# Optimization experiments

Measured on AMD Instinct MI355X. Metric: run time of the kernel, lower is better.

Reference implementation:

```python
import jax, jax.numpy as jnp
import numpy as np

N = 100000   # num nodes
E = 1200000  # num edges
D = 64       # embedding dim
K = 3        # propagation hops (alpha has K+1 entries)


def setup_inputs() -> dict:
    key = jax.random.key(0)
    k1, k2, k3 = jax.random.split(key, 3)
    edge_index = jax.random.randint(k1, (2, E), 0, N, dtype=jnp.int64)
    weight = jax.random.normal(k2, (N, D), dtype=jnp.float32)
    alpha = jax.random.uniform(k3, (K + 1,), dtype=jnp.float32)
    return {"edge_index": edge_index, "weight": weight, "alpha": alpha}


def reference(edge_index, weight, alpha):
    row = edge_index[0]  # source j
    col = edge_index[1]  # target i
    # symmetric normalization: in-degree over col, deg^-1/2 with inf -> 0
    deg = jax.ops.segment_sum(jnp.ones((E,), dtype=weight.dtype), col, num_segments=N)
    dinv = jnp.where(deg == 0, 0.0, deg ** -0.5)
    edge_w = dinv[row] * dinv[col]  # [E]

    out = weight * alpha[0]
    x = weight
    for k in range(1, K + 1):
        # gather-scale-scatter propagation hop
        msg = edge_w[:, None] * x[row]                      # [E, D]
        x = jax.ops.segment_sum(msg, col, num_segments=N)   # [N, D]
        out = out + x * alpha[k]

    # per-edge link scores: dot(out[src], out[dst])
    return jnp.sum(out[row] * out[col], axis=-1)  # [E]
```

## Files before the change

### kernel.cpp

```cpp
#include <hip/hip_runtime.h>
#include <hip/hip_bf16.h>

#define GN 100000
#define GE 1200000
#define GD 64
#define NG 256
#define CPG 391
#define CAP 6144
#define PADCAP 12032
#define ZROFF (GN << 7)


__global__ void detect_kernel(const void* __restrict__ w,
                              const void* __restrict__ edge,
                              int* __restrict__ flags, int* __restrict__ gcount,
                              __hip_bfloat16* __restrict__ X,
                              __hip_bfloat16* __restrict__ Y) {
    __shared__ int s_badw, s_edgenz;
    if (threadIdx.x == 0) { s_badw = 0; s_edgenz = 0; }
    gcount[threadIdx.x] = 0;
    if (threadIdx.x < 16) {
        uint2 z; z.x = 0u; z.y = 0u;
        *(uint2*)(X + (size_t)GN * GD + 4 * threadIdx.x) = z;
        *(uint2*)(Y + (size_t)GN * GD + 4 * threadIdx.x) = z;
    }
    __syncthreads();
    const unsigned short* wh = (const unsigned short*)w;
    const unsigned int*   ei = (const unsigned int*)edge;
    int badw = 0, edgenz = 0;
    for (int i = threadIdx.x; i < 4096; i += 256) {
        unsigned int bits = ((unsigned int)wh[i]) << 16;
        float v = __uint_as_float(bits);
        if (!(fabsf(v) <= 100.0f)) badw = 1;
        if ((i & 1) == 1 && ei[i] != 0u) edgenz = 1;
    }
    if (badw)   atomicOr(&s_badw, 1);
    if (edgenz) atomicOr(&s_edgenz, 1);
    __syncthreads();
    if (threadIdx.x == 0) {
        flags[0] = s_badw ? 0 : 1;
        flags[1] = s_edgenz ? 0 : 1;
    }
}

__device__ __forceinline__ int ld_row(const int* __restrict__ edge, int e, int e64) {
    return e64 ? edge[2 * (size_t)e] : edge[e];
}
__device__ __forceinline__ int ld_col(const int* __restrict__ edge, int e, int e64) {
    return e64 ? edge[2 * ((size_t)GE + (size_t)e)] : edge[(size_t)GE + (size_t)e];
}
__device__ __forceinline__ float ld_f(const void* __restrict__ p, size_t i, int bf16f) {
    if (bf16f) return __bfloat162float(((const __hip_bfloat16*)p)[i]);
    return ((const float*)p)[i];
}

__device__ __forceinline__ float bf_lo(unsigned u) { return __uint_as_float(u << 16); }
__device__ __forceinline__ float bf_hi(unsigned u) { return __uint_as_float(u & 0xFFFF0000u); }
__device__ __forceinline__ unsigned bf16bits(float f) {
    __hip_bfloat16 h = __float2bfloat16(f);
    unsigned short s;
    __builtin_memcpy(&s, &h, 2);
    return (unsigned)s;
}

__global__ void p1init_kernel(const int* __restrict__ edge, const int* __restrict__ flags,
                              int* __restrict__ gcount, unsigned* __restrict__ bucket,
                              int E, int chunk,
                              const void* __restrict__ w, const void* __restrict__ alpha,
                              __hip_bfloat16* __restrict__ OUT, int nd) {
    if (blockIdx.x < NG) {
        __shared__ int cnt[NG];
        __shared__ int base[NG];
        int t = threadIdx.x;
        int e64 = flags[1];
        cnt[t] = 0;
        __syncthreads();
        int lo = blockIdx.x * chunk;
        int hiE = min(lo + chunk, E);
        for (int e = lo + t; e < hiE; e += 256) {
            int c = ld_col(edge, e, e64);
            int r = ld_row(edge, e, e64);
            if ((unsigned)c < (unsigned)GN && (unsigned)r < (unsigned)GN)
                atomicAdd(&cnt[c / CPG], 1);
        }
        __syncthreads();
        int cv = cnt[t];
        base[t] = (cv > 0) ? atomicAdd(&gcount[t], cv) : 0;
        __syncthreads();
        cnt[t] = 0;
        __syncthreads();
        for (int e = lo + t; e < hiE; e += 256) {
            int c = ld_col(edge, e, e64);
            int r = ld_row(edge, e, e64);
            if ((unsigned)c < (unsigned)GN && (unsigned)r < (unsigned)GN) {
                int g = c / CPG;
                int idx = base[g] + atomicAdd(&cnt[g], 1);
                if (idx < CAP)
                    bucket[(size_t)g * CAP + idx] = ((unsigned)(c - g * CPG) << 17) | (unsigned)r;
            }
        }
    } else {
        int bid = blockIdx.x - NG;
        int i = 4 * (bid * 256 + (int)threadIdx.x);
        int wbf = flags[0];
        if (i < nd) {
            float a0 = ld_f(alpha, 0, wbf);
            float v0 = ld_f(w, i + 0, wbf);
            float v1 = ld_f(w, i + 1, wbf);
            float v2 = ld_f(w, i + 2, wbf);
            float v3 = ld_f(w, i + 3, wbf);
            uint2 oq;
            oq.x = (bf16bits(a0 * v1) << 16) | bf16bits(a0 * v0);
            oq.y = (bf16bits(a0 * v3) << 16) | bf16bits(a0 * v2);
            *(uint2*)(OUT + i) = oq;
        }
    }
}

__global__ void p2_kernel(const unsigned* __restrict__ bucket, const int* __restrict__ gcount,
                          int2* __restrict__ begend, float* __restrict__ dinv,
                          int* __restrict__ csr,
                          const void* __restrict__ w, const int* __restrict__ flags,
                          __hip_bfloat16* __restrict__ XS) {
    int g = blockIdx.x;
    int t = threadIdx.x;
    __shared__ int hist[512];
    __shared__ int s[512];
    __shared__ float sdv[512];
    hist[t] = 0; hist[t + 256] = 0;
    __syncthreads();
    int mg = gcount[g]; if (mg > CAP) mg = CAP;
    const unsigned* bk = bucket + (size_t)g * CAP;
    for (int idx = t; idx < mg; idx += 256)
        atomicAdd(&hist[bk[idx] >> 17], 1);
    __syncthreads();
    int h0 = hist[t], h1 = hist[t + 256];
    int p0 = (h0 + 15) & ~15;
    int p1 = (h1 + 15) & ~15;
    s[t] = p0; s[t + 256] = p1;
    __syncthreads();
    for (int off = 1; off < 512; off <<= 1) {
        int v0 = (t >= off) ? s[t - off] : 0;
        int v1 = (t + 256 >= off) ? s[t + 256 - off] : 0;
        __syncthreads();
        s[t] += v0; s[t + 256] += v1;
        __syncthreads();
    }
    int gb = g * PADCAP;
    int beg0 = gb + s[t] - p0;
    int beg1 = gb + s[t + 256] - p1;
    float dv0 = (h0 > 0) ? rsqrtf((float)h0) : 0.0f;
    float dv1 = (h1 > 0) ? rsqrtf((float)h1) : 0.0f;
    sdv[t] = dv0; sdv[t + 256] = dv1;
    int col0 = g * CPG + t;
    int col1 = col0 + 256;
    if (col0 < GN) {
        begend[col0] = make_int2(beg0, beg0 + p0);
        dinv[col0] = dv0;
    }
    if (t + 256 < CPG && col1 < GN) {
        begend[col1] = make_int2(beg1, beg1 + p1);
        dinv[col1] = dv1;
    }
    __syncthreads();
    hist[t] = s[t] - p0;
    hist[t + 256] = s[t + 256] - p1;
    __syncthreads();
    for (int idx = t; idx < mg; idx += 256) {
        unsigned u = bk[idx];
        int cl = u >> 17;
        int r  = (int)(u & 0x1FFFFu);
        int pos = gb + atomicAdd(&hist[cl], 1);
        csr[pos] = r << 7;
    }
    if (col0 < GN)
        for (int q = h0; q < p0; ++q) csr[beg0 + q] = ZROFF;
    if (t + 256 < CPG && col1 < GN)
        for (int q = h1; q < p1; ++q) csr[beg1 + q] = ZROFF;
    int lo = g * CPG;
    int ncols = min(CPG, GN - lo);
    int tot = ncols << 6;
    int wbf = flags[0];
    size_t gbase = (size_t)lo << 6;
    if (wbf) {
        const unsigned short* wp = (const unsigned short*)w;
        for (int idx = 4 * t; idx < tot; idx += 1024) {
            float dv = sdv[idx >> 6];
            size_t base = gbase + (size_t)idx;
            uint2 wv = *(const uint2*)(wp + base);
            uint2 o;
            o.x = (bf16bits(dv * bf_hi(wv.x)) << 16) | bf16bits(dv * bf_lo(wv.x));
            o.y = (bf16bits(dv * bf_hi(wv.y)) << 16) | bf16bits(dv * bf_lo(wv.y));
            *(uint2*)(XS + base) = o;
        }
    } else {
        const float* wp = (const float*)w;
        for (int idx = 4 * t; idx < tot; idx += 1024) {
            float dv = sdv[idx >> 6];
            size_t base = gbase + (size_t)idx;
            float4 wv = *(const float4*)(wp + base);
            uint2 o;
            o.x = (bf16bits(dv * wv.y) << 16) | bf16bits(dv * wv.x);
            o.y = (bf16bits(dv * wv.w) << 16) | bf16bits(dv * wv.z);
            *(uint2*)(XS + base) = o;
        }
    }
}

__global__ void gather_kernel(const __hip_bfloat16* __restrict__ XS,
                              __hip_bfloat16* __restrict__ Y,
                              __hip_bfloat16* __restrict__ OUT,
                              const int2* __restrict__ begend, const int* __restrict__ csr,
                              const float* __restrict__ dinv,
                              const void* __restrict__ alpha, const int* __restrict__ flags,
                              int k, int store_y, int N) {
    int t = blockIdx.x * blockDim.x + threadIdx.x;
    int node = __builtin_amdgcn_readfirstlane(t >> 6);
    if (node >= N) return;
    int lane = t & 63;
    int h = lane >> 4;
    int i = lane & 15;
    int2 be = begend[node];
    int beg = be.x, end = be.y;
    float dc = dinv[node];
    float a = ld_f(alpha, k, flags[0]);
    size_t obase = (size_t)node * GD + 4 * i;
    uint2 uo = *(const uint2*)(OUT + obase);
    const char* xb = (const char*)XS;
    unsigned ioff = 8u * (unsigned)i;
    float f0 = 0.0f, f1 = 0.0f, f2 = 0.0f, f3 = 0.0f;
    for (int j = beg; j < end; j += 16) {
        int rv = csr[j + i];
        unsigned r0 = (unsigned)__shfl(rv, h,      16);
        unsigned r1 = (unsigned)__shfl(rv, 4 + h,  16);
        unsigned r2 = (unsigned)__shfl(rv, 8 + h,  16);
        unsigned r3 = (unsigned)__shfl(rv, 12 + h, 16);
        uint2 u0 = *(const uint2*)(xb + (r0 + ioff));
        uint2 u1 = *(const uint2*)(xb + (r1 + ioff));
        uint2 u2 = *(const uint2*)(xb + (r2 + ioff));
        uint2 u3 = *(const uint2*)(xb + (r3 + ioff));
        f0 += bf_lo(u0.x); f1 += bf_hi(u0.x); f2 += bf_lo(u0.y); f3 += bf_hi(u0.y);
        f0 += bf_lo(u1.x); f1 += bf_hi(u1.x); f2 += bf_lo(u1.y); f3 += bf_hi(u1.y);
        f0 += bf_lo(u2.x); f1 += bf_hi(u2.x); f2 += bf_lo(u2.y); f3 += bf_hi(u2.y);
        f0 += bf_lo(u3.x); f1 += bf_hi(u3.x); f2 += bf_lo(u3.y); f3 += bf_hi(u3.y);
    }
    f0 += __shfl_xor(f0, 16, 64); f0 += __shfl_xor(f0, 32, 64);
    f1 += __shfl_xor(f1, 16, 64); f1 += __shfl_xor(f1, 32, 64);
    f2 += __shfl_xor(f2, 16, 64); f2 += __shfl_xor(f2, 32, 64);
    f3 += __shfl_xor(f3, 16, 64); f3 += __shfl_xor(f3, 32, 64);
    f0 *= dc; f1 *= dc; f2 *= dc; f3 *= dc;
    if (h == 0) {
        if (store_y) {
            uint2 p;
            p.x = (bf16bits(dc * f1) << 16) | bf16bits(dc * f0);
            p.y = (bf16bits(dc * f3) << 16) | bf16bits(dc * f2);
            *(uint2*)(Y + obase) = p;
        }
        float o0 = fmaf(a, f0, bf_lo(uo.x));
        float o1 = fmaf(a, f1, bf_hi(uo.x));
        float o2 = fmaf(a, f2, bf_lo(uo.y));
        float o3 = fmaf(a, f3, bf_hi(uo.y));
        uint2 q;
        q.x = (bf16bits(o1) << 16) | bf16bits(o0);
        q.y = (bf16bits(o3) << 16) | bf16bits(o2);
        *(uint2*)(OUT + obase) = q;
    }
}

__device__ __forceinline__ float dot2_bf16(unsigned ua, unsigned ub) {
    return fmaf(bf_lo(ua), bf_lo(ub), bf_hi(ua) * bf_hi(ub));
}

__global__ void dot_kernel(const __hip_bfloat16* __restrict__ OUT,
                           const int* __restrict__ edge, const int* __restrict__ flags,
                           void* __restrict__ res, int E) {
    int t = blockIdx.x * blockDim.x + threadIdx.x;
    int e = t >> 2;
    int sub = t & 3;
    if (e >= E) return;
    int e64 = flags[1];
    int wbf = flags[0];
    int r = ld_row(edge, e, e64);
    int c = ld_col(edge, e, e64);
    float p = 0.0f;
    if ((unsigned)r < (unsigned)GN && (unsigned)c < (unsigned)GN) {
        const uint4* pa = (const uint4*)(OUT + (size_t)r * GD + sub * 16);
        const uint4* pb = (const uint4*)(OUT + (size_t)c * GD + sub * 16);
        uint4 a0 = pa[0], a1 = pa[1];
        uint4 b0 = pb[0], b1 = pb[1];
        p = ((dot2_bf16(a0.x, b0.x) + dot2_bf16(a0.y, b0.y)) +
             (dot2_bf16(a0.z, b0.z) + dot2_bf16(a0.w, b0.w))) +
            ((dot2_bf16(a1.x, b1.x) + dot2_bf16(a1.y, b1.y)) +
             (dot2_bf16(a1.z, b1.z) + dot2_bf16(a1.w, b1.w)));
    }
    p += __shfl_down(p, 2, 4);
    p += __shfl_down(p, 1, 4);
    if (sub == 0) {
        if (wbf) ((__hip_bfloat16*)res)[e] = __float2bfloat16(p);
        else     ((float*)res)[e] = p;
    }
}

extern "C" void kernel_launch(void* const* d_in, const int* in_sizes, int n_in,
                              void* d_out, int out_size, void* d_ws, size_t ws_size,
                              hipStream_t stream) {
    const int E = GE, N = GN, ND = GN * GD;
    const int NDP = (GN + 1) * GD;

    const void* edge   = d_in[0];
    const void* weight = d_in[1];
    const void* alpha  = d_in[2];

    char* ws = (char*)d_ws;
    int*      flags     = (int*)ws;      ws += 256;
    int*      gcount    = (int*)ws;      ws += 1024;
    float*    dinv      = (float*)ws;    ws += (((size_t)N * 4 + 255) / 256) * 256;
    int2*     begend    = (int2*)ws;     ws += (((size_t)N * 8 + 255) / 256) * 256;
    unsigned* bucket    = (unsigned*)ws; ws += (size_t)NG * CAP * 4;
    int*      csr       = (int*)ws;      ws += (size_t)NG * PADCAP * 4;
    __hip_bfloat16* X   = (__hip_bfloat16*)ws; ws += (size_t)NDP * 2;
    __hip_bfloat16* Y   = (__hip_bfloat16*)ws; ws += (size_t)NDP * 2;
    __hip_bfloat16* OUT = (__hip_bfloat16*)ws; ws += (size_t)ND * 2;

    const int B = 256;

    detect_kernel<<<1, 256, 0, stream>>>(weight, edge, flags, gcount, X, Y);

    {
        const int chunk = (E + NG - 1) / NG;
        const int initBlocks = (ND / 4 + B - 1) / B;
        p1init_kernel<<<NG + initBlocks, B, 0, stream>>>(
            (const int*)edge, flags, gcount, bucket, E, chunk,
            weight, alpha, OUT, ND);
    }
    p2_kernel<<<NG, 256, 0, stream>>>(bucket, gcount, begend, dinv, csr,
                                      weight, flags, X);

    const int ggrid = (int)(((size_t)N * 64 + B - 1) / B);
    gather_kernel<<<ggrid, B, 0, stream>>>(X, Y, OUT, begend, csr, dinv, alpha, flags, 1, 1, N);
    gather_kernel<<<ggrid, B, 0, stream>>>(Y, X, OUT, begend, csr, dinv, alpha, flags, 2, 1, N);
    gather_kernel<<<ggrid, B, 0, stream>>>(X, Y, OUT, begend, csr, dinv, alpha, flags, 3, 0, N);

    dot_kernel<<<(int)(((size_t)E * 4 + B - 1) / B), B, 0, stream>>>(OUT, (const int*)edge, flags, d_out, E);
}
```

Measured before the change: 259.0 us.

## Convert gather and dot kernels to persistent grid-stride loops with software prefetch

Gather and dot kernels now launch a fixed grid of 2048 blocks. Each wave loops over several nodes or edges with a grid stride instead of handling one. Inside the loop, the next item's CSR bounds, dinv, OUT row, first index chunk and edge endpoints with their embedding rows are prefetched while the current item is being reduced, to hide gather latency. The cost is more registers per thread and less parallelism per launch. The dot kernel also switches from a bounds branch to masked clamped loads.

```diff
diff --git a/kernel.cpp b/kernel.cpp
--- a/kernel.cpp
+++ b/kernel.cpp
@@ -207,63 +207,88 @@
     }
 }
 
+__device__ __forceinline__ void acc16(int rv, unsigned ioff, const char* __restrict__ xb,
+                                      int h, float& f0, float& f1, float& f2, float& f3) {
+    unsigned r0 = (unsigned)__shfl(rv, h,      16);
+    unsigned r1 = (unsigned)__shfl(rv, 4 + h,  16);
+    unsigned r2 = (unsigned)__shfl(rv, 8 + h,  16);
+    unsigned r3 = (unsigned)__shfl(rv, 12 + h, 16);
+    uint2 u0 = *(const uint2*)(xb + (r0 + ioff));
+    uint2 u1 = *(const uint2*)(xb + (r1 + ioff));
+    uint2 u2 = *(const uint2*)(xb + (r2 + ioff));
+    uint2 u3 = *(const uint2*)(xb + (r3 + ioff));
+    f0 += bf_lo(u0.x); f1 += bf_hi(u0.x); f2 += bf_lo(u0.y); f3 += bf_hi(u0.y);
+    f0 += bf_lo(u1.x); f1 += bf_hi(u1.x); f2 += bf_lo(u1.y); f3 += bf_hi(u1.y);
+    f0 += bf_lo(u2.x); f1 += bf_hi(u2.x); f2 += bf_lo(u2.y); f3 += bf_hi(u2.y);
+    f0 += bf_lo(u3.x); f1 += bf_hi(u3.x); f2 += bf_lo(u3.y); f3 += bf_hi(u3.y);
+}
+
 __global__ void gather_kernel(const __hip_bfloat16* __restrict__ XS,
                               __hip_bfloat16* __restrict__ Y,
                               __hip_bfloat16* __restrict__ OUT,
                               const int2* __restrict__ begend, const int* __restrict__ csr,
                               const float* __restrict__ dinv,
                               const void* __restrict__ alpha, const int* __restrict__ flags,
-                              int k, int store_y, int N) {
+                              int k, int store_y, int N, int W) {
     int t = blockIdx.x * blockDim.x + threadIdx.x;
-    int node = __builtin_amdgcn_readfirstlane(t >> 6);
-    if (node >= N) return;
+    int wid = __builtin_amdgcn_readfirstlane(t >> 6);
+    if (wid >= N) return;
     int lane = t & 63;
     int h = lane >> 4;
     int i = lane & 15;
+    float a = ld_f(alpha, k, flags[0]);
+    const char* xb = (const char*)XS;
+    unsigned ioff = 8u * (unsigned)i;
+    int node = wid;
     int2 be = begend[node];
-    int beg = be.x, end = be.y;
     float dc = dinv[node];
-    float a = ld_f(alpha, k, flags[0]);
     size_t obase = (size_t)node * GD + 4 * i;
     uint2 uo = *(const uint2*)(OUT + obase);
-    const char* xb = (const char*)XS;
-    unsigned ioff = 8u * (unsigned)i;
-    float f0 = 0.0f, f1 = 0.0f, f2 = 0.0f, f3 = 0.0f;
-    for (int j = beg; j < end; j += 16) {
-        int rv = csr[j + i];
-        unsigned r0 = (unsigned)__shfl(rv, h,      16);
-        unsigned r1 = (unsigned)__shfl(rv, 4 + h,  16);
-        unsigned r2 = (unsigned)__shfl(rv, 8 + h,  16);
-        unsigned r3 = (unsigned)__shfl(rv, 12 + h, 16);
-        uint2 u0 = *(const uint2*)(xb + (r0 + ioff));
-        uint2 u1 = *(const uint2*)(xb + (r1 + ioff));
-        uint2 u2 = *(const uint2*)(xb + (r2 + ioff));
-        uint2 u3 = *(const uint2*)(xb + (r3 + ioff));
-        f0 += bf_lo(u0.x); f1 += bf_hi(u0.x); f2 += bf_lo(u0.y); f3 += bf_hi(u0.y);
-        f0 += bf_lo(u1.x); f1 += bf_hi(u1.x); f2 += bf_lo(u1.y); f3 += bf_hi(u1.y);
-        f0 += bf_lo(u2.x); f1 += bf_hi(u2.x); f2 += bf_lo(u2.y); f3 += bf_hi(u2.y);
-        f0 += bf_lo(u3.x); f1 += bf_hi(u3.x); f2 += bf_lo(u3.y); f3 += bf_hi(u3.y);
-    }
-    f0 += __shfl_xor(f0, 16, 64); f0 += __shfl_xor(f0, 32, 64);
-    f1 += __shfl_xor(f1, 16, 64); f1 += __shfl_xor(f1, 32, 64);
-    f2 += __shfl_xor(f2, 16, 64); f2 += __shfl_xor(f2, 32, 64);
-    f3 += __shfl_xor(f3, 16, 64); f3 += __shfl_xor(f3, 32, 64);
-    f0 *= dc; f1 *= dc; f2 *= dc; f3 *= dc;
-    if (h == 0) {
-        if (store_y) {
-            uint2 p;
-            p.x = (bf16bits(dc * f1) << 16) | bf16bits(dc * f0);
-            p.y = (bf16bits(dc * f3) << 16) | bf16bits(dc * f2);
-            *(uint2*)(Y + obase) = p;
-        }
-        float o0 = fmaf(a, f0, bf_lo(uo.x));
-        float o1 = fmaf(a, f1, bf_hi(uo.x));
-        float o2 = fmaf(a, f2, bf_lo(uo.y));
-        float o3 = fmaf(a, f3, bf_hi(uo.y));
-        uint2 q;
-        q.x = (bf16bits(o1) << 16) | bf16bits(o0);
-        q.y = (bf16bits(o3) << 16) | bf16bits(o2);
-        *(uint2*)(OUT + obase) = q;
+    int rv = csr[be.x + i];
+    for (;;) {
+        int nn = node + W;
+        bool more = nn < N;
+        int2 be_n = make_int2(0, 0);
+        float dc_n = 0.0f;
+        uint2 uo_n; uo_n.x = 0u; uo_n.y = 0u;
+        int rv_n = 0;
+        if (more) {
+            be_n = begend[nn];
+            dc_n = dinv[nn];
+            uo_n = *(const uint2*)(OUT + (size_t)nn * GD + 4 * i);
+        }
+        float f0 = 0.0f, f1 = 0.0f, f2 = 0.0f, f3 = 0.0f;
+        int j = be.x;
+        if (j < be.y) {
+            acc16(rv, ioff, xb, h, f0, f1, f2, f3);
+            for (j += 16; j < be.y; j += 16)
+                acc16(csr[j + i], ioff, xb, h, f0, f1, f2, f3);
+        }
+        if (more) rv_n = csr[be_n.x + i];
+        f0 += __shfl_xor(f0, 16, 64); f0 += __shfl_xor(f0, 32, 64);
+        f1 += __shfl_xor(f1, 16, 64); f1 += __shfl_xor(f1, 32, 64);
+        f2 += __shfl_xor(f2, 16, 64); f2 += __shfl_xor(f2, 32, 64);
+        f3 += __shfl_xor(f3, 16, 64); f3 += __shfl_xor(f3, 32, 64);
+        f0 *= dc; f1 *= dc; f2 *= dc; f3 *= dc;
+        if (h == 0) {
+            if (store_y) {
+                uint2 p;
+                p.x = (bf16bits(dc * f1) << 16) | bf16bits(dc * f0);
+                p.y = (bf16bits(dc * f3) << 16) | bf16bits(dc * f2);
+                *(uint2*)(Y + obase) = p;
+            }
+            float o0 = fmaf(a, f0, bf_lo(uo.x));
+            float o1 = fmaf(a, f1, bf_hi(uo.x));
+            float o2 = fmaf(a, f2, bf_lo(uo.y));
+            float o3 = fmaf(a, f3, bf_hi(uo.y));
+            uint2 q;
+            q.x = (bf16bits(o1) << 16) | bf16bits(o0);
+            q.y = (bf16bits(o3) << 16) | bf16bits(o2);
+            *(uint2*)(OUT + obase) = q;
+        }
+        if (!more) break;
+        node = nn; be = be_n; dc = dc_n; uo = uo_n; rv = rv_n;
+        obase = (size_t)node * GD + 4 * i;
     }
 }
 
@@ -273,31 +298,56 @@
 
 __global__ void dot_kernel(const __hip_bfloat16* __restrict__ OUT,
                            const int* __restrict__ edge, const int* __restrict__ flags,
-                           void* __restrict__ res, int E) {
+                           void* __restrict__ res, int E, int NQ) {
     int t = blockIdx.x * blockDim.x + threadIdx.x;
-    int e = t >> 2;
+    int q = t >> 2;
     int sub = t & 3;
-    if (e >= E) return;
+    if (q >= E) return;
     int e64 = flags[1];
     int wbf = flags[0];
-    int r = ld_row(edge, e, e64);
-    int c = ld_col(edge, e, e64);
-    float p = 0.0f;
-    if ((unsigned)r < (unsigned)GN && (unsigned)c < (unsigned)GN) {
-        const uint4* pa = (const uint4*)(OUT + (size_t)r * GD + sub * 16);
-        const uint4* pb = (const uint4*)(OUT + (size_t)c * GD + sub * 16);
-        uint4 a0 = pa[0], a1 = pa[1];
-        uint4 b0 = pb[0], b1 = pb[1];
-        p = ((dot2_bf16(a0.x, b0.x) + dot2_bf16(a0.y, b0.y)) +
-             (dot2_bf16(a0.z, b0.z) + dot2_bf16(a0.w, b0.w))) +
-            ((dot2_bf16(a1.x, b1.x) + dot2_bf16(a1.y, b1.y)) +
-             (dot2_bf16(a1.z, b1.z) + dot2_bf16(a1.w, b1.w)));
-    }
-    p += __shfl_down(p, 2, 4);
-    p += __shfl_down(p, 1, 4);
-    if (sub == 0) {
-        if (wbf) ((__hip_bfloat16*)res)[e] = __float2bfloat16(p);
-        else     ((float*)res)[e] = p;
+    int e0 = q;
+    int r0 = ld_row(edge, e0, e64);
+    int c0 = ld_col(edge, e0, e64);
+    float m0 = ((unsigned)r0 < (unsigned)GN && (unsigned)c0 < (unsigned)GN) ? 1.0f : 0.0f;
+    unsigned rc = ((unsigned)r0 < (unsigned)GN) ? (unsigned)r0 : 0u;
+    unsigned cc = ((unsigned)c0 < (unsigned)GN) ? (unsigned)c0 : 0u;
+    const uint4* pa = (const uint4*)(OUT + (size_t)rc * GD + sub * 16);
+    const uint4* pb = (const uint4*)(OUT + (size_t)cc * GD + sub * 16);
+    uint4 a0 = pa[0], a1 = pa[1], b0 = pb[0], b1 = pb[1];
+    int e1 = e0 + NQ;
+    bool more1 = e1 < E;
+    int r1 = 0, c1 = 0;
+    if (more1) { r1 = ld_row(edge, e1, e64); c1 = ld_col(edge, e1, e64); }
+    for (;;) {
+        uint4 na0, na1, nb0, nb1;
+        na0.x=na0.y=na0.z=na0.w=0u; na1=na0; nb0=na0; nb1=na0;
+        float m1 = 0.0f;
+        if (more1) {
+            m1 = ((unsigned)r1 < (unsigned)GN && (unsigned)c1 < (unsigned)GN) ? 1.0f : 0.0f;
+            unsigned rc1 = ((unsigned)r1 < (unsigned)GN) ? (unsigned)r1 : 0u;
+            unsigned cc1 = ((unsigned)c1 < (unsigned)GN) ? (unsigned)c1 : 0u;
+            const uint4* qa = (const uint4*)(OUT + (size_t)rc1 * GD + sub * 16);
+            const uint4* qb = (const uint4*)(OUT + (size_t)cc1 * GD + sub * 16);
+            na0 = qa[0]; na1 = qa[1]; nb0 = qb[0]; nb1 = qb[1];
+        }
+        int e2 = e1 + NQ;
+        bool more2 = more1 && (e2 < E);
+        int r2 = 0, c2 = 0;
+        if (more2) { r2 = ld_row(edge, e2, e64); c2 = ld_col(edge, e2, e64); }
+        float p = (((dot2_bf16(a0.x, b0.x) + dot2_bf16(a0.y, b0.y)) +
+                    (dot2_bf16(a0.z, b0.z) + dot2_bf16(a0.w, b0.w))) +
+                   ((dot2_bf16(a1.x, b1.x) + dot2_bf16(a1.y, b1.y)) +
+                    (dot2_bf16(a1.z, b1.z) + dot2_bf16(a1.w, b1.w)))) * m0;
+        p += __shfl_down(p, 2, 4);
+        p += __shfl_down(p, 1, 4);
+        if (sub == 0) {
+            if (wbf) ((__hip_bfloat16*)res)[e0] = __float2bfloat16(p);
+            else     ((float*)res)[e0] = p;
+        }
+        if (!more1) break;
+        e0 = e1; m0 = m1;
+        a0 = na0; a1 = na1; b0 = nb0; b1 = nb1;
+        e1 = e2; more1 = more2; r1 = r2; c1 = c2;
     }
 }
 
@@ -336,10 +386,12 @@
     p2_kernel<<<NG, 256, 0, stream>>>(bucket, gcount, begend, dinv, csr,
                                       weight, flags, X);
 
-    const int ggrid = (int)(((size_t)N * 64 + B - 1) / B);
-    gather_kernel<<<ggrid, B, 0, stream>>>(X, Y, OUT, begend, csr, dinv, alpha, flags, 1, 1, N);
-    gather_kernel<<<ggrid, B, 0, stream>>>(Y, X, OUT, begend, csr, dinv, alpha, flags, 2, 1, N);
-    gather_kernel<<<ggrid, B, 0, stream>>>(X, Y, OUT, begend, csr, dinv, alpha, flags, 3, 0, N);
-
-    dot_kernel<<<(int)(((size_t)E * 4 + B - 1) / B), B, 0, stream>>>(OUT, (const int*)edge, flags, d_out, E);
-}
+    const int PB = 2048;
+    const int W  = PB * (B / 64);
+    gather_kernel<<<PB, B, 0, stream>>>(X, Y, OUT, begend, csr, dinv, alpha, flags, 1, 1, N, W);
+    gather_kernel<<<PB, B, 0, stream>>>(Y, X, OUT, begend, csr, dinv, alpha, flags, 2, 1, N, W);
+    gather_kernel<<<PB, B, 0, stream>>>(X, Y, OUT, begend, csr, dinv, alpha, flags, 3, 0, N, W);
+
+    const int NQ = PB * B / 4;
+    dot_kernel<<<PB, B, 0, stream>>>(OUT, (const int*)edge, flags, d_out, E, NQ);
+}
```

After: 245.3 us. 1.06x faster.
